# Kernel tuning notes

Measured on AMD Instinct MI355X. Metric: run time of the kernel, lower is better.

The kernel has to match this reference:

```python
import jax, jax.numpy as jnp
import numpy as np

S, P = 64, 32          # scenes, pedestrians per scene (uniform)
N = S * P              # total pedestrians = 2048
H, E = 64, 64          # h_dim, embedding_dim
D1, D2 = 512, 1024     # mlp_pre_pool hidden, bottleneck_dim
EPS = 1e-5             # torch BatchNorm1d eps


def _batchnorm(x, gamma, beta):
    # Training-mode BN with per-scene batch stats (matches the per-scene
    # loop in the original, where BN sees one scene's num_ped^2 rows).
    # x: [S, P*P, D]
    mu = jnp.mean(x, axis=1, keepdims=True)
    var = jnp.mean(jnp.square(x - mu), axis=1, keepdims=True)  # biased var, as torch BN
    return (x - mu) * jax.lax.rsqrt(var + EPS) * gamma + beta


def setup_inputs() -> dict:
    key = jax.random.key(0)
    ks = jax.random.split(key, 16)
    h_states = jax.random.normal(ks[0], (1, N, H), jnp.float32)
    starts = jnp.arange(S, dtype=jnp.int32) * P
    seq_start_end = jnp.stack([starts, starts + P], axis=1)  # [S, 2]
    end_pos = jax.random.normal(ks[1], (N, 2), jnp.float32)
    rel_pos = jax.random.normal(ks[2], (N, 2), jnp.float32)  # unused (pooling_dim=2) but a fwd arg
    sc = 0.05
    params = dict(
        W_embed=jax.random.normal(ks[3], (2, E), jnp.float32) * sc,
        b_embed=jnp.zeros((E,), jnp.float32),
        W1=jax.random.normal(ks[4], (E + H, D1), jnp.float32) * sc,
        b1=jnp.zeros((D1,), jnp.float32),
        g1=jnp.ones((D1,), jnp.float32),
        be1=jnp.zeros((D1,), jnp.float32),
        W2=jax.random.normal(ks[5], (D1, D2), jnp.float32) * sc,
        b2=jnp.zeros((D2,), jnp.float32),
        g2=jnp.ones((D2,), jnp.float32),
        be2=jnp.zeros((D2,), jnp.float32),
    )
    return dict(h_states=h_states, seq_start_end=seq_start_end,
                end_pos=end_pos, rel_pos=rel_pos, **params)


def reference(h_states, seq_start_end, end_pos, rel_pos,
              W_embed, b_embed, W1, b1, g1, be1, W2, b2, g2, be2):
    # Uniform scenes: seq_start_end delimits S contiguous blocks of P peds.
    pos = end_pos.reshape(S, P, 2)
    h = h_states.reshape(N, H).reshape(S, P, H)
    # Original indexing: row (k*P + j) -> pos[j] - pos[k], hidden[j];
    # the final view(P, P, -1).max(1) maxes over j for each k.
    rel = pos[:, None, :, :] - pos[:, :, None, :]          # [S, Pk, Pj, 2]
    emb = rel @ W_embed + b_embed                          # [S, Pk, Pj, E]
    hid = jnp.broadcast_to(h[:, None, :, :], (S, P, P, H)) # hidden of j
    x = jnp.concatenate([emb, hid], axis=-1).reshape(S, P * P, E + H)
    x = jax.nn.relu(_batchnorm(x @ W1 + b1, g1, be1))      # [S, P*P, 512]
    x = jax.nn.relu(_batchnorm(x @ W2 + b2, g2, be2))      # [S, P*P, 1024]
    pool_h = x.reshape(S, P, P, D2).max(axis=2)            # max over j
    return pool_h.reshape(N, D2)
```

## Files before the change

kernel.cpp:

```cpp
#include <hip/hip_runtime.h>
#include <hip/hip_bf16.h>

#define S_ 64
#define P_ 32
#define N_ 2048
#define H_ 64
#define E_ 64
#define D1_ 512
#define D2_ 1024
#define EPS_ 1e-5f

typedef unsigned short u16;
using bf16x8 = __attribute__((ext_vector_type(8))) __bf16;
using floatx4 = __attribute__((ext_vector_type(4))) float;

__device__ inline u16 f2bf(float x) {
    unsigned u = __float_as_uint(x);
    unsigned r = (u + 0x7fffu + ((u >> 16) & 1u)) >> 16;
    return (u16)r;
}


__device__ void prep_scene_256(int u, int tid, float* smem,
                               const float* __restrict__ pos, const float* __restrict__ h,
                               const float* __restrict__ We, const float* __restrict__ W1,
                               const float* __restrict__ g1, const float* __restrict__ be1,
                               float* __restrict__ A, float* __restrict__ Bv) {
    const int s = u >> 2, dq = u & 3;
    const int jg = tid >> 7, dl = tid & 127;
    const int d = (dq << 7) + dl;
    float* hs = smem;
    float* ps = smem + 2048;
    float* red = smem + 2112;
    for (int i = tid; i < 2048; i += 256) hs[i] = h[(size_t)s * 2048 + i];
    if (tid < 64) ps[tid] = pos[s * 64 + tid];
    __syncthreads();
    float wq0 = 0.f, wq1 = 0.f;
    for (int e = 0; e < 64; ++e) {
        const float wv = W1[e * 512 + d];
        wq0 += We[e] * wv;
        wq1 += We[64 + e] * wv;
    }
    float w[16], uu[16];
#pragma unroll
    for (int jj = 0; jj < 16; ++jj) w[jj] = 0.f;
    const float4* h4 = (const float4*)hs;
    for (int e4 = 0; e4 < 16; ++e4) {
        const float c0 = W1[(64 + e4 * 4 + 0) * 512 + d];
        const float c1 = W1[(64 + e4 * 4 + 1) * 512 + d];
        const float c2 = W1[(64 + e4 * 4 + 2) * 512 + d];
        const float c3 = W1[(64 + e4 * 4 + 3) * 512 + d];
#pragma unroll
        for (int jj = 0; jj < 16; ++jj) {
            const float4 hv = h4[((jg << 4) + jj) * 16 + e4];
            w[jj] += hv.x * c0 + hv.y * c1 + hv.z * c2 + hv.w * c3;
        }
    }
    float sw = 0.f, sww = 0.f, su = 0.f, suu = 0.f;
#pragma unroll
    for (int jj = 0; jj < 16; ++jj) {
        const int j = (jg << 4) + jj;
        uu[jj] = ps[2 * j] * wq0 + ps[2 * j + 1] * wq1;
        w[jj] += uu[jj];
        sw += w[jj]; sww += w[jj] * w[jj];
        su += uu[jj]; suu += uu[jj] * uu[jj];
    }
    red[(jg << 7) + dl] = sw;
    red[256 + (jg << 7) + dl] = sww;
    red[512 + (jg << 7) + dl] = su;
    red[768 + (jg << 7) + dl] = suu;
    __syncthreads();
    const float tw = red[dl] + red[128 + dl];
    const float tww = red[256 + dl] + red[384 + dl];
    const float tu = red[512 + dl] + red[640 + dl];
    const float tuu = red[768 + dl] + red[896 + dl];
    const float mw = tw * (1.f / 32.f), mu2 = tu * (1.f / 32.f);
    const float var = (tww * (1.f / 32.f) - mw * mw) + (tuu * (1.f / 32.f) - mu2 * mu2);
    const float sc = rsqrtf(var + EPS_) * g1[d];
    const float bb = be1[d];
#pragma unroll
    for (int jj = 0; jj < 16; ++jj) {
        const int j = (jg << 4) + jj;
        A[(size_t)(s * 32 + j) * 512 + d] = (w[jj] - mw) * sc + bb;
        Bv[(size_t)(s * 32 + j) * 512 + d] = (uu[jj] - mu2) * sc;
    }
}

__device__ void w2t_tile_256(int b2, int tid, void* smem,
                             const float* __restrict__ W2, u16* __restrict__ w2t) {
    float (*tile)[65] = (float (*)[65])smem;
    const int bi = b2 & 15, bj = b2 >> 4;
    const int tx = tid & 63, ty = tid >> 6;
#pragma unroll
    for (int i = 0; i < 64; i += 4)
        tile[ty + i][tx] = W2[(size_t)(bj * 64 + ty + i) * 1024 + bi * 64 + tx];
    __syncthreads();
#pragma unroll
    for (int i = 0; i < 64; i += 4)
        w2t[(size_t)(bi * 64 + ty + i) * 512 + bj * 64 + tx] = f2bf(tile[tx][ty + i]);
}


__device__ __forceinline__ void ld4x4(float4 d[4], const float* __restrict__ p) {
    d[0] = *(const float4*)(p);
    d[1] = *(const float4*)(p + 4);
    d[2] = *(const float4*)(p + 8);
    d[3] = *(const float4*)(p + 12);
}

__device__ __forceinline__ void build_half(u16* __restrict__ AsN, int rowb,
                                           int posA, int posB,
                                           const float4 a[4], const float4 b[4]) {
    bf16x8 o;
    o[0] = (__bf16)fmaxf(a[0].x - b[0].x, 0.f);
    o[1] = (__bf16)fmaxf(a[0].y - b[0].y, 0.f);
    o[2] = (__bf16)fmaxf(a[0].z - b[0].z, 0.f);
    o[3] = (__bf16)fmaxf(a[0].w - b[0].w, 0.f);
    o[4] = (__bf16)fmaxf(a[1].x - b[1].x, 0.f);
    o[5] = (__bf16)fmaxf(a[1].y - b[1].y, 0.f);
    o[6] = (__bf16)fmaxf(a[1].z - b[1].z, 0.f);
    o[7] = (__bf16)fmaxf(a[1].w - b[1].w, 0.f);
    *(bf16x8*)(AsN + rowb + posA) = o;
    bf16x8 p;
    p[0] = (__bf16)fmaxf(a[2].x - b[2].x, 0.f);
    p[1] = (__bf16)fmaxf(a[2].y - b[2].y, 0.f);
    p[2] = (__bf16)fmaxf(a[2].z - b[2].z, 0.f);
    p[3] = (__bf16)fmaxf(a[2].w - b[2].w, 0.f);
    p[4] = (__bf16)fmaxf(a[3].x - b[3].x, 0.f);
    p[5] = (__bf16)fmaxf(a[3].y - b[3].y, 0.f);
    p[6] = (__bf16)fmaxf(a[3].z - b[3].z, 0.f);
    p[7] = (__bf16)fmaxf(a[3].w - b[3].w, 0.f);
    *(bf16x8*)(AsN + rowb + posB) = p;
}

__device__ __forceinline__ void stage_ws(const u16* __restrict__ w2t, u16* WsN,
                                         int N0, int kcol, int h, int wave,
                                         int lrow, int gchk) {
#pragma unroll
    for (int c = 0; c < 2; ++c) {
        const int rbase = h * 128 + wave * 16 + c * 8;
        const u16* gb = w2t + (size_t)(N0 + rbase + lrow) * 512 + kcol + gchk * 8;
        __builtin_amdgcn_global_load_lds(
            (const __attribute__((address_space(1))) void*)gb,
            (__attribute__((address_space(3))) void*)(WsN + rbase * 64), 16, 0, 0);
    }
}

template <int QM, int QN>
__device__ __forceinline__ void read_frags(bf16x8 af[4], bf16x8 wf[2],
                                           const u16* __restrict__ Ab,
                                           const u16* __restrict__ Wb,
                                           int wm, int wn, int l16, int pos) {
#pragma unroll
    for (int i = 0; i < 4; ++i)
        af[i] = *(const bf16x8*)(Ab + (wm * 128 + (QM * 4 + i) * 16 + l16) * 64 + pos);
#pragma unroll
    for (int n = 0; n < 2; ++n)
        wf[n] = *(const bf16x8*)(Wb + (wn * 64 + (QN * 2 + n) * 16 + l16) * 64 + pos);
}

template <int QM, int QN>
__device__ __forceinline__ void do_mfma(floatx4 (&acc)[8][4],
                                        const bf16x8 af[4], const bf16x8 wf[2]) {
#pragma unroll
    for (int i = 0; i < 4; ++i)
#pragma unroll
        for (int n = 0; n < 2; ++n)
            acc[QM * 4 + i][QN * 2 + n] = __builtin_amdgcn_mfma_f32_16x16x32_bf16(
                af[i], wf[n], acc[QM * 4 + i][QN * 2 + n], 0, 0, 0);
}

#define LGKM0() asm volatile("s_waitcnt lgkmcnt(0)" ::: "memory")
#define VM0()   asm volatile("s_waitcnt vmcnt(0)" ::: "memory")

__global__ __launch_bounds__(512, 2)
void k_gemm(const float* __restrict__ A, const float* __restrict__ Bv,
            const u16* __restrict__ w2t,
            float* __restrict__ maxv, float* __restrict__ minv,
            float* __restrict__ psum, float* __restrict__ psumsq) {
    extern __shared__ __align__(16) char lds_raw[];
    u16* AsB = (u16*)lds_raw;
    u16* WsB = AsB + 32768;

    const int tid = threadIdx.x;
    const int wave = tid >> 6, lane = tid & 63;
    const int wm = wave >> 2, wn = wave & 3;
    const int quad = lane >> 4, l16 = lane & 15;
    const int lrow = lane >> 3, gchk = (lane & 7) ^ lrow;

    const int bid = blockIdx.x;
    const int mb = bid >> 2, nb = bid & 3;
    const int s = mb >> 2, kq = mb & 3;
    const int N0 = nb << 8;

    const int brow = tid >> 2, kq4 = tid & 3;
    const int j0 = brow & 31, pl0 = brow >> 5;
    const float* Arow = A + ((size_t)(s * 32 + j0) << 9) + (kq4 << 4);
    const float* Brow0 = Bv + ((size_t)(s * 32 + kq * 8 + pl0) << 9) + (kq4 << 4);
    const float* Brow1 = Brow0 + (4 << 9);
    const int posA = ((kq4 * 2) ^ (brow & 7)) << 3;
    const int posB = ((kq4 * 2 + 1) ^ (brow & 7)) << 3;
    const int rowb0 = brow * 64;
    const int rowb1 = (128 + brow) * 64;

    const int posk0 = ((quad) ^ (l16 & 7)) << 3;
    const int posk1 = ((4 + quad) ^ (l16 & 7)) << 3;

    floatx4 acc[8][4] = {};

    {
        float4 xa[4], xb[4], yb[4];
        ld4x4(xa, Arow); ld4x4(xb, Brow0); ld4x4(yb, Brow1);
        stage_ws(w2t, WsB, N0, 0, 0, wave, lrow, gchk);
        stage_ws(w2t, WsB, N0, 0, 1, wave, lrow, gchk);
        build_half(AsB, rowb0, posA, posB, xa, xb);
        build_half(AsB, rowb1, posA, posB, xa, yb);
        LGKM0();
        VM0();
        __builtin_amdgcn_s_barrier();
    }

    for (int t = 0; t < 8; ++t) {
        const int buf = t & 1;
        const u16* Ab = AsB + (buf << 14);
        const u16* Wb = WsB + (buf << 14);
        u16* AsN = AsB + ((buf ^ 1) << 14);
        u16* WsN = WsB + ((buf ^ 1) << 14);
        const bool pf = (t < 7);
        const int kn = (t + 1) << 6;

        float4 xa[4], xb[4], yb[4];

        {
            bf16x8 af[4], wf[2];
            read_frags<0, 0>(af, wf, Ab, Wb, wm, wn, l16, posk0);
            if (pf) { ld4x4(xa, Arow + kn); ld4x4(xb, Brow0 + kn); }
            LGKM0();
            __builtin_amdgcn_s_barrier();
            __builtin_amdgcn_s_setprio(1);
            do_mfma<0, 0>(acc, af, wf);
            read_frags<0, 0>(af, wf, Ab, Wb, wm, wn, l16, posk1);
            do_mfma<0, 0>(acc, af, wf);
            __builtin_amdgcn_s_setprio(0);
        }
        {
            bf16x8 af[4], wf[2];
            read_frags<0, 1>(af, wf, Ab, Wb, wm, wn, l16, posk0);
            if (pf) {
                stage_ws(w2t, WsN, N0, kn, 0, wave, lrow, gchk);
                ld4x4(yb, Brow1 + kn);
                build_half(AsN, rowb0, posA, posB, xa, xb);
            }
            LGKM0();
            __builtin_amdgcn_s_barrier();
            __builtin_amdgcn_s_setprio(1);
            do_mfma<0, 1>(acc, af, wf);
            read_frags<0, 1>(af, wf, Ab, Wb, wm, wn, l16, posk1);
            do_mfma<0, 1>(acc, af, wf);
            __builtin_amdgcn_s_setprio(0);
        }
        {
            bf16x8 af[4], wf[2];
            read_frags<1, 0>(af, wf, Ab, Wb, wm, wn, l16, posk0);
            if (pf) {
                stage_ws(w2t, WsN, N0, kn, 1, wave, lrow, gchk);
                build_half(AsN, rowb1, posA, posB, xa, yb);
            }
            LGKM0();
            __builtin_amdgcn_s_barrier();
            __builtin_amdgcn_s_setprio(1);
            do_mfma<1, 0>(acc, af, wf);
            read_frags<1, 0>(af, wf, Ab, Wb, wm, wn, l16, posk1);
            do_mfma<1, 0>(acc, af, wf);
            __builtin_amdgcn_s_setprio(0);
        }
        {
            bf16x8 af[4], wf[2];
            read_frags<1, 1>(af, wf, Ab, Wb, wm, wn, l16, posk0);
            LGKM0();
            if (pf) VM0();
            __builtin_amdgcn_s_barrier();
            __builtin_amdgcn_s_setprio(1);
            do_mfma<1, 1>(acc, af, wf);
            read_frags<1, 1>(af, wf, Ab, Wb, wm, wn, l16, posk1);
            do_mfma<1, 1>(acc, af, wf);
            __builtin_amdgcn_s_setprio(0);
        }
    }

#pragma unroll
    for (int tn = 0; tn < 4; ++tn) {
        const int col = N0 + wn * 64 + tn * 16 + l16;
        float wsum = 0.f, wsq = 0.f;
#pragma unroll
        for (int e = 0; e < 4; ++e) {
            float vmax = -3.4e38f, vmin = 3.4e38f, vs = 0.f, vq = 0.f;
#pragma unroll
            for (int tm = e * 2; tm < e * 2 + 2; ++tm)
#pragma unroll
                for (int r = 0; r < 4; ++r) {
                    const float v = acc[tm][tn][r];
                    vmax = fmaxf(vmax, v);
                    vmin = fminf(vmin, v);
                    vs += v;
                    vq += v * v;
                }
#pragma unroll
            for (int off = 16; off < 64; off <<= 1) {
                vmax = fmaxf(vmax, __shfl_xor(vmax, off));
                vmin = fminf(vmin, __shfl_xor(vmin, off));
                vs += __shfl_xor(vs, off);
                vq += __shfl_xor(vq, off);
            }
            if (quad == 0) {
                const int kg = s * 32 + kq * 8 + wm * 4 + e;
                maxv[(size_t)kg * 1024 + col] = vmax;
                minv[(size_t)kg * 1024 + col] = vmin;
            }
            wsum += vs;
            wsq += vq;
        }
        if (quad == 0) {
            const int slot = ((s * 4 + kq) << 1) + wm;
            psum[(size_t)slot * 1024 + col] = wsum;
            psumsq[(size_t)slot * 1024 + col] = wsq;
        }
    }
}

__global__ __launch_bounds__(256)
void k_prep(const float* __restrict__ pos, const float* __restrict__ h,
            const float* __restrict__ We, const float* __restrict__ W1,
            const float* __restrict__ g1, const float* __restrict__ be1,
            const float* __restrict__ W2,
            float* __restrict__ A, float* __restrict__ Bv, u16* __restrict__ w2t) {
    __shared__ __align__(16) char smem_raw[16912];
    const int bid = blockIdx.x;
    if (bid < 256)
        prep_scene_256(bid, threadIdx.x, (float*)smem_raw, pos, h, We, W1, g1, be1, A, Bv);
    else
        w2t_tile_256(bid - 256, threadIdx.x, smem_raw, W2, w2t);
}

__global__ __launch_bounds__(256)
void k_final(const float* __restrict__ maxv, const float* __restrict__ minv,
             const float* __restrict__ psum, const float* __restrict__ psumsq,
             const float* __restrict__ g2, const float* __restrict__ be2,
             float* __restrict__ out) {
    const int u = blockIdx.x, tid = threadIdx.x;
    const int s3 = u >> 2;
    const int c = ((u & 3) << 8) + tid;
    float sm = 0.f, sq = 0.f;
#pragma unroll
    for (int t = 0; t < 8; ++t) {
        sm += psum[(size_t)(s3 * 8 + t) * 1024 + c];
        sq += psumsq[(size_t)(s3 * 8 + t) * 1024 + c];
    }
    const float mu = sm * (1.f / 1024.f);
    const float var = sq * (1.f / 1024.f) - mu * mu;
    const float inv = rsqrtf(var + EPS_);
    const float scale = g2[c] * inv;
    const float bb = be2[c];
    const float* src = (scale >= 0.f) ? maxv : minv;
    for (int k = 0; k < 32; ++k) {
        const float v = src[(size_t)(s3 * 32 + k) * 1024 + c];
        out[(size_t)(s3 * 32 + k) * 1024 + c] = fmaxf((v - mu) * scale + bb, 0.f);
    }
}

extern "C" void kernel_launch(void* const* d_in, const int* in_sizes, int n_in,
                              void* d_out, int out_size, void* d_ws, size_t ws_size,
                              hipStream_t stream) {
    const float* h_states = (const float*)d_in[0];
    const float* end_pos = (const float*)d_in[2];
    const float* W_embed = (const float*)d_in[4];
    const float* W1 = (const float*)d_in[6];
    const float* g1 = (const float*)d_in[8];
    const float* be1 = (const float*)d_in[9];
    const float* W2 = (const float*)d_in[10];
    const float* g2 = (const float*)d_in[12];
    const float* be2 = (const float*)d_in[13];
    float* out = (float*)d_out;

    float* Abuf = (float*)d_ws;
    float* Bbuf = Abuf + 1048576;
    float* maxv = Bbuf + 1048576;
    float* minv = maxv + 2097152;
    float* psum = minv + 2097152;
    float* psumsq = psum + 1048576;
    u16* w2t = (u16*)(psumsq + 1048576);

    static int lds_opt_in = 0;
    if (!lds_opt_in) {
        hipFuncSetAttribute(reinterpret_cast<const void*>(k_gemm),
                            hipFuncAttributeMaxDynamicSharedMemorySize, 131072);
        lds_opt_in = 1;
    }

    k_prep<<<dim3(384), dim3(256), 0, stream>>>(end_pos, h_states, W_embed, W1,
                                                g1, be1, W2, Abuf, Bbuf, w2t);
    k_gemm<<<dim3(1024), dim3(512), 131072, stream>>>(Abuf, Bbuf, w2t, maxv, minv,
                                                      psum, psumsq);
    k_final<<<dim3(256), dim3(256), 0, stream>>>(maxv, minv, psum, psumsq, g2, be2, out);
}
```

Measured before the change: 216.3 us.

## Prefetch A/B global tiles two K-steps ahead and restructure barrier sandwich

Global register loads of the A/B fp32 rows now run two K-steps ahead, so each build into LDS uses data fetched a full iteration earlier. Partial vmcnt waits (vmcnt(12)) let the newest loads stay in flight across the boundary instead of draining everything. Both weight stages are issued at the top of each iteration, and every MFMA block is bracketed by barriers in a macro. This hides global latency better, at the cost of more live registers, an extra barrier per phase, and reliance on exact vmcnt counting being correct.

```diff
diff --git a/kernel.cpp b/kernel.cpp
--- a/kernel.cpp
+++ b/kernel.cpp
@@ -172,6 +172,17 @@
 
 #define LGKM0() asm volatile("s_waitcnt lgkmcnt(0)" ::: "memory")
 #define VM0()   asm volatile("s_waitcnt vmcnt(0)" ::: "memory")
+#define VMC12() asm volatile("s_waitcnt vmcnt(12)" ::: "memory")
+
+#define SANDWICH(QM, QN)                                              \
+    __builtin_amdgcn_s_barrier();                                     \
+    LGKM0();                                                          \
+    __builtin_amdgcn_s_setprio(1);                                    \
+    do_mfma<QM, QN>(acc, af, wf);                                     \
+    read_frags<QM, QN>(af, wf, Ab, Wb, wm, wn, l16, posk1);           \
+    do_mfma<QM, QN>(acc, af, wf);                                     \
+    __builtin_amdgcn_s_setprio(0);                                    \
+    __builtin_amdgcn_s_barrier();
 
 __global__ __launch_bounds__(512, 2)
 void k_gemm(const float* __restrict__ A, const float* __restrict__ Bv,
@@ -207,16 +218,17 @@
     const int posk1 = ((4 + quad) ^ (l16 & 7)) << 3;
 
     floatx4 acc[8][4] = {};
+    float4 xa[4], xb[4], yb[4];
 
     {
-        float4 xa[4], xb[4], yb[4];
         ld4x4(xa, Arow); ld4x4(xb, Brow0); ld4x4(yb, Brow1);
         stage_ws(w2t, WsB, N0, 0, 0, wave, lrow, gchk);
         stage_ws(w2t, WsB, N0, 0, 1, wave, lrow, gchk);
         build_half(AsB, rowb0, posA, posB, xa, xb);
         build_half(AsB, rowb1, posA, posB, xa, yb);
+        ld4x4(xa, Arow + 64); ld4x4(xb, Brow0 + 64); ld4x4(yb, Brow1 + 64);
+        VMC12();
         LGKM0();
-        VM0();
         __builtin_amdgcn_s_barrier();
     }
 
@@ -228,64 +240,32 @@
         u16* WsN = WsB + ((buf ^ 1) << 14);
         const bool pf = (t < 7);
         const int kn = (t + 1) << 6;
-
-        float4 xa[4], xb[4], yb[4];
-
-        {
-            bf16x8 af[4], wf[2];
-            read_frags<0, 0>(af, wf, Ab, Wb, wm, wn, l16, posk0);
-            if (pf) { ld4x4(xa, Arow + kn); ld4x4(xb, Brow0 + kn); }
-            LGKM0();
-            __builtin_amdgcn_s_barrier();
-            __builtin_amdgcn_s_setprio(1);
-            do_mfma<0, 0>(acc, af, wf);
-            read_frags<0, 0>(af, wf, Ab, Wb, wm, wn, l16, posk1);
-            do_mfma<0, 0>(acc, af, wf);
-            __builtin_amdgcn_s_setprio(0);
-        }
-        {
-            bf16x8 af[4], wf[2];
-            read_frags<0, 1>(af, wf, Ab, Wb, wm, wn, l16, posk0);
-            if (pf) {
-                stage_ws(w2t, WsN, N0, kn, 0, wave, lrow, gchk);
-                ld4x4(yb, Brow1 + kn);
-                build_half(AsN, rowb0, posA, posB, xa, xb);
-            }
-            LGKM0();
-            __builtin_amdgcn_s_barrier();
-            __builtin_amdgcn_s_setprio(1);
-            do_mfma<0, 1>(acc, af, wf);
-            read_frags<0, 1>(af, wf, Ab, Wb, wm, wn, l16, posk1);
-            do_mfma<0, 1>(acc, af, wf);
-            __builtin_amdgcn_s_setprio(0);
-        }
-        {
-            bf16x8 af[4], wf[2];
-            read_frags<1, 0>(af, wf, Ab, Wb, wm, wn, l16, posk0);
-            if (pf) {
-                stage_ws(w2t, WsN, N0, kn, 1, wave, lrow, gchk);
-                build_half(AsN, rowb1, posA, posB, xa, yb);
-            }
-            LGKM0();
-            __builtin_amdgcn_s_barrier();
-            __builtin_amdgcn_s_setprio(1);
-            do_mfma<1, 0>(acc, af, wf);
-            read_frags<1, 0>(af, wf, Ab, Wb, wm, wn, l16, posk1);
-            do_mfma<1, 0>(acc, af, wf);
-            __builtin_amdgcn_s_setprio(0);
-        }
-        {
-            bf16x8 af[4], wf[2];
-            read_frags<1, 1>(af, wf, Ab, Wb, wm, wn, l16, posk0);
-            LGKM0();
-            if (pf) VM0();
-            __builtin_amdgcn_s_barrier();
-            __builtin_amdgcn_s_setprio(1);
-            do_mfma<1, 1>(acc, af, wf);
-            read_frags<1, 1>(af, wf, Ab, Wb, wm, wn, l16, posk1);
-            do_mfma<1, 1>(acc, af, wf);
-            __builtin_amdgcn_s_setprio(0);
-        }
+        bf16x8 af[4], wf[2];
+
+        if (pf) {
+            stage_ws(w2t, WsN, N0, kn, 0, wave, lrow, gchk);
+            stage_ws(w2t, WsN, N0, kn, 1, wave, lrow, gchk);
+        }
+        read_frags<0, 0>(af, wf, Ab, Wb, wm, wn, l16, posk0);
+        SANDWICH(0, 0)
+
+        if (pf) build_half(AsN, rowb0, posA, posB, xa, xb);
+        read_frags<0, 1>(af, wf, Ab, Wb, wm, wn, l16, posk0);
+        SANDWICH(0, 1)
+
+        if (pf) build_half(AsN, rowb1, posA, posB, xa, yb);
+        read_frags<1, 0>(af, wf, Ab, Wb, wm, wn, l16, posk0);
+        SANDWICH(1, 0)
+
+        if (t < 6) {
+            const int kn2 = (t + 2) << 6;
+            ld4x4(xa, Arow + kn2); ld4x4(xb, Brow0 + kn2); ld4x4(yb, Brow1 + kn2);
+            VMC12();
+        } else {
+            VM0();
+        }
+        read_frags<1, 1>(af, wf, Ab, Wb, wm, wn, l16, posk0);
+        SANDWICH(1, 1)
     }
 
 #pragma unroll
```

After: 211.0 us. 1.02x faster.
